# Performance work log

Hardware: AMD Instinct MI355X
Metric: run time of the kernel (lower is better)

The kernel has to match this reference:

```python
import jax, jax.numpy as jnp
import numpy as np


def setup_inputs() -> dict:
    key = jax.random.key(0)
    k1, k2, k3 = jax.random.split(key, 3)
    B, S, D, N = 2, 2048, 1024, 16
    H = D // N  # head_dim = 64
    x = jax.random.normal(k1, (B, S, D), dtype=jnp.float32)
    W_qkv = jax.random.normal(k2, (N, D, 3 * H), dtype=jnp.float32) / np.sqrt(D).astype(np.float32)
    W_out = jax.random.normal(k3, (N, H, D), dtype=jnp.float32) / np.sqrt(D).astype(np.float32)
    return {"x": x, "W_qkv": W_qkv, "W_out": W_out}


def reference(x, W_qkv, W_out):
    B, S, D = x.shape
    head_dim = W_qkv.shape[-1] // 3
    # QKV projection per head: [B, N, S, 3*H]
    qkv = jnp.einsum('bsd,ndh->bnsh', x, W_qkv)
    q, k, v = jnp.split(qkv, 3, axis=-1)  # each [B, N, S, H]
    scale = jnp.asarray(1.0 / np.sqrt(head_dim), dtype=x.dtype)
    attn = jnp.einsum('bnqh,bnkh->bnqk', q, k) * scale  # [B, N, S, S]
    # causal mask: -1e10 above the diagonal (matches buffer in original)
    mask = jnp.asarray(-1e10, dtype=x.dtype) * (1.0 - jnp.tril(jnp.ones((S, S), dtype=x.dtype)))
    attn = jax.nn.softmax(attn + mask, axis=-1)
    out = jnp.einsum('bnqk,bnkh->bnqh', attn, v)  # [B, N, S, H]
    # faithful to original: raw row-major reshape [B,N,S,H] -> [B, N*H, S]
    out = out.reshape(B, -1, S)
    # faithful to original einsum: d kept, n and h summed over W_out
    return jnp.einsum('bds,nhd->bsd', out, W_out)
```

## Files before the change

### kernel.cpp

```cpp
#include <hip/hip_runtime.h>
#include <hip/hip_bf16.h>

#define B_ 2
#define S_ 2048
#define D_ 1024
#define N_ 16
#define H_ 64

typedef unsigned short u16;
typedef unsigned int u32;
typedef __bf16 bf16x8 __attribute__((ext_vector_type(8)));
typedef u16 u16x8 __attribute__((ext_vector_type(8)));
typedef u32 u32x2 __attribute__((ext_vector_type(2)));
typedef float f4v __attribute__((ext_vector_type(4)));

__device__ __forceinline__ u16 f2b(float f) {
    u32 u = __builtin_bit_cast(u32, f);
    u32 r = (u + 0x7FFFu + ((u >> 16) & 1u)) >> 16;
    return (u16)r;
}
__device__ __forceinline__ bf16x8 asbf(u16x8 v) { return __builtin_bit_cast(bf16x8, v); }
__device__ __forceinline__ u32 cvtpk(float a, float b) {
    u32 r;
    asm("v_cvt_pk_bf16_f32 %0, %1, %2" : "=v"(r) : "v"(a), "v"(b));
    return r;
}
__device__ __forceinline__ void gload16(const u16* g, u16* l) {
    __builtin_amdgcn_global_load_lds((const __attribute__((address_space(1))) void*)g,
                                     (__attribute__((address_space(3))) void*)l, 16, 0, 0);
}

__global__ __launch_bounds__(256) void k_setup(const float* __restrict__ x,
                                               const float* __restrict__ w,
                                               const float* __restrict__ Wout,
                                               u16* __restrict__ xb,
                                               u16* __restrict__ wt,
                                               float* __restrict__ wsum) {
    __shared__ float T[64][65];
    const int bid = blockIdx.x;
    const int t = threadIdx.x;
    if (bid < 2048) {
        size_t i = ((size_t)bid * 256 + t) * 8;
        float4 f0 = *(const float4*)(x + i);
        float4 f1 = *(const float4*)(x + i + 4);
        u16x8 o;
        o[0] = f2b(f0.x); o[1] = f2b(f0.y); o[2] = f2b(f0.z); o[3] = f2b(f0.w);
        o[4] = f2b(f1.x); o[5] = f2b(f1.y); o[6] = f2b(f1.z); o[7] = f2b(f1.w);
        *(u16x8*)(xb + i) = o;
    } else if (bid < 2816) {
        const int v = bid - 2048;
        const int n = v / 48, rem = v % 48;
        const int jt = rem >> 4, d0 = (rem & 15) * 64;
        const int j0 = jt * 64;
        const float sc = (jt == 0) ? 0.125f * 1.44269504089f : 1.0f;
#pragma unroll
        for (int rep = 0; rep < 4; ++rep) {
            int vv = t + rep * 256;
            int row = vv >> 4, c4 = vv & 15;
            float4 f = *(const float4*)(w + ((size_t)(n * 1024 + d0 + row)) * 192 + j0 + c4 * 4);
            T[row][c4 * 4 + 0] = f.x * sc;
            T[row][c4 * 4 + 1] = f.y * sc;
            T[row][c4 * 4 + 2] = f.z * sc;
            T[row][c4 * 4 + 3] = f.w * sc;
        }
        __syncthreads();
#pragma unroll
        for (int rep = 0; rep < 2; ++rep) {
            int c = t + rep * 256;
            int j = c >> 3, db = c & 7;
            u16x8 o;
#pragma unroll
            for (int e = 0; e < 8; ++e) o[e] = f2b(T[db * 8 + e][j]);
            *(u16x8*)(wt + ((size_t)(n * 192 + j0 + j)) * 1024 + d0 + db * 8) = o;
        }
    } else {
        const int bx = bid - 2816;
        const int dd = t & 15, rr = t >> 4;
        const int d = bx * 16 + dd;
        float s = 0.f;
        for (int r = rr * 64; r < rr * 64 + 64; ++r) s += Wout[(size_t)r * 1024 + d];
        float* red = &T[0][0];
        red[rr * 17 + dd] = s;
        __syncthreads();
        if (rr == 0) {
            float tt = 0.f;
#pragma unroll
            for (int k = 0; k < 16; ++k) tt += red[k * 17 + dd];
            wsum[d] = tt;
        }
    }
}

__global__ __launch_bounds__(512) void k_qkv(const u16* __restrict__ xb,
                                             const u16* __restrict__ wt,
                                             u16* __restrict__ qbuf,
                                             u16* __restrict__ kbuf,
                                             u16* __restrict__ vt) {
    __shared__ u16 As[128 * 64];
    __shared__ u16 Bst[192 * 64];
    const int st = blockIdx.x, n = blockIdx.y;
    const int t = threadIdx.x;
    const int w = t >> 6, lane = t & 63, hi2 = lane >> 4, lo4 = lane & 15;
    const int wm = w >> 2, wn = w & 3;

    const int l8 = lane >> 3, l7 = (lane & 7) * 8;
    const u16* AgL = xb + (size_t)(st * 128 + w * 16 + l8) * 1024 + l7;
    u16* AdL = As + w * 16 * 64;
    const u16* BgL = wt + (size_t)(n * 192 + w * 24 + l8) * 1024 + l7;
    u16* BdL = Bst + w * 24 * 64;

    f4v acc[4][3];
#pragma unroll
    for (int i = 0; i < 4; ++i)
#pragma unroll
        for (int j = 0; j < 3; ++j) acc[i][j] = (f4v){0.f, 0.f, 0.f, 0.f};

    for (int kk = 0; kk < 16; ++kk) {
        __syncthreads();
        const int ko = kk * 64;
        gload16(AgL + ko, AdL);
        gload16(AgL + ko + (size_t)8 * 1024, AdL + 8 * 64);
        gload16(BgL + ko, BdL);
        gload16(BgL + ko + (size_t)8 * 1024, BdL + 8 * 64);
        gload16(BgL + ko + (size_t)16 * 1024, BdL + 16 * 64);
        __syncthreads();
        bf16x8 fa[4][2];
#pragma unroll
        for (int ms = 0; ms < 4; ++ms) {
            const u16* ar = As + (wm * 64 + ms * 16 + lo4) * 64;
            fa[ms][0] = asbf(*(const u16x8*)(ar + hi2 * 8));
            fa[ms][1] = asbf(*(const u16x8*)(ar + hi2 * 8 + 32));
        }
        __builtin_amdgcn_s_setprio(1);
#pragma unroll
        for (int fj = 0; fj < 3; ++fj) {
            const u16* br = Bst + (wn * 48 + fj * 16 + lo4) * 64;
            bf16x8 fb0 = asbf(*(const u16x8*)(br + hi2 * 8));
            bf16x8 fb1 = asbf(*(const u16x8*)(br + hi2 * 8 + 32));
#pragma unroll
            for (int ms = 0; ms < 4; ++ms) {
                acc[ms][fj] = __builtin_amdgcn_mfma_f32_16x16x32_bf16(fa[ms][0], fb0, acc[ms][fj], 0, 0, 0);
                acc[ms][fj] = __builtin_amdgcn_mfma_f32_16x16x32_bf16(fa[ms][1], fb1, acc[ms][fj], 0, 0, 0);
            }
        }
        __builtin_amdgcn_s_setprio(0);
    }

    const int b = st >> 4, s128 = (st & 15) * 128;
    u16* Cs = As;
#pragma unroll
    for (int sec = 0; sec < 3; ++sec) {
        __syncthreads();
#pragma unroll
        for (int fj = 0; fj < 3; ++fj) {
            const int base = wn * 48 + fj * 16;
            if ((base >> 6) == sec) {
                const int col = base - sec * 64 + lo4;
#pragma unroll
                for (int ms = 0; ms < 4; ++ms)
#pragma unroll
                    for (int r = 0; r < 4; ++r)
                        Cs[(wm * 64 + ms * 16 + hi2 * 4 + r) * 64 + col] = f2b(acc[ms][fj][r]);
            }
        }
        __syncthreads();
        if (sec == 2) {
            const int h = t & 63, sb = t >> 6;
            u16x8 o0, o1;
#pragma unroll
            for (int e = 0; e < 8; ++e) o0[e] = Cs[(sb * 16 + e) * 64 + h];
#pragma unroll
            for (int e = 0; e < 8; ++e) o1[e] = Cs[(sb * 16 + 8 + e) * 64 + h];
            u16* dst = vt + ((size_t)(b * 16 + n) * 64 + h) * 2048 + s128 + sb * 16;
            *(u16x8*)dst = o0;
            *(u16x8*)(dst + 8) = o1;
        } else {
            const int row = t >> 2, off = (t & 3) * 16;
            u16* dst = (sec == 0) ? qbuf : kbuf;
            dst += ((size_t)(b * 16 + n) * 2048 + s128 + row) * 64 + off;
            *(u16x8*)dst = *(const u16x8*)(Cs + row * 64 + off);
            *(u16x8*)(dst + 8) = *(const u16x8*)(Cs + row * 64 + off + 8);
        }
    }
}

__global__ __launch_bounds__(512) void k_attn(const u16* __restrict__ qbuf,
                                              const u16* __restrict__ kbuf,
                                              const u16* __restrict__ vt,
                                              const float* __restrict__ wsum,
                                              float* __restrict__ out) {
    __shared__ u16 SMEM[24576];
    u16* Ks = SMEM;
    u16* Vs = SMEM + 8192;
    u16* Ps = SMEM + 16384;
    const int id = blockIdx.x;
    const int bn = id & 31;
    const int qx = id >> 5;
    const int qb = (qx < 8) ? (15 - 2 * qx) : (2 * (qx - 8));
    const int t = threadIdx.x;
    const int w = t >> 6, lane = t & 63, hi2 = lane >> 4, lo4 = lane & 15;

    const int q = qb * 128 + w * 16 + lo4;
    const u16* Qp = qbuf + ((size_t)bn * 2048 + q) * 64;
    bf16x8 bq0 = asbf(*(const u16x8*)(Qp + hi2 * 8));
    bf16x8 bq1 = asbf(*(const u16x8*)(Qp + 32 + hi2 * 8));

    const int srow = t >> 3, so = t & 7;
    const u16* Kg = kbuf + (size_t)bn * 2048 * 64 + (size_t)srow * 64 + so * 8;
    const u16* Vg = vt + (size_t)bn * 64 * 2048 + (size_t)srow * 2048 + so * 8;
    const int soff = srow * 64 + ((so * 8) ^ ((srow & 7) << 3));

    f4v accO[4];
#pragma unroll
    for (int i = 0; i < 4; ++i) accO[i] = (f4v){0.f, 0.f, 0.f, 0.f};
    float l = 0.f;

    const int rsw = (lo4 & 7) << 3;
    u16* Pw = Ps + w * 1024 + lo4 * 64;
    const int npair = qb + 1;

    u16x8 krA = *(const u16x8*)(Kg);
    u16x8 krB = *(const u16x8*)(Kg + 4096);
    u16x8 vrA = *(const u16x8*)(Vg);
    u16x8 vrB = *(const u16x8*)(Vg + 64);

    for (int pair = 0; pair < npair; ++pair) {
        __syncthreads();
        *(u16x8*)(Ks + soff) = krA;
        *(u16x8*)(Ks + 4096 + soff) = krB;
        *(u16x8*)(Vs + soff) = vrA;
        *(u16x8*)(Vs + 4096 + soff) = vrB;
        if (pair + 1 < npair) {
            const size_t ko = (size_t)(pair + 1) * 8192;
            krA = *(const u16x8*)(Kg + ko);
            krB = *(const u16x8*)(Kg + ko + 4096);
            vrA = *(const u16x8*)(Vg + (pair + 1) * 128);
            vrB = *(const u16x8*)(Vg + (pair + 1) * 128 + 64);
        }
        __syncthreads();

#pragma unroll
        for (int sub = 0; sub < 2; ++sub) {
            const int kb = 2 * pair + sub;
            const u16* Kc = Ks + sub * 4096;
            const u16* Vc = Vs + sub * 4096;

            f4v s4[4];
#pragma unroll
            for (int i = 0; i < 4; ++i) s4[i] = (f4v){0.f, 0.f, 0.f, 0.f};
            __builtin_amdgcn_s_setprio(1);
#pragma unroll
            for (int fi = 0; fi < 4; ++fi) {
                const u16* kr = Kc + (fi * 16 + lo4) * 64;
                bf16x8 ka0 = asbf(*(const u16x8*)(kr + ((hi2 * 8) ^ rsw)));
                bf16x8 ka1 = asbf(*(const u16x8*)(kr + ((hi2 * 8 + 32) ^ rsw)));
                s4[fi] = __builtin_amdgcn_mfma_f32_16x16x32_bf16(ka0, bq0, s4[fi], 0, 0, 0);
                s4[fi] = __builtin_amdgcn_mfma_f32_16x16x32_bf16(ka1, bq1, s4[fi], 0, 0, 0);
            }
            __builtin_amdgcn_s_setprio(0);

            if (kb >= 2 * qb) {
#pragma unroll
                for (int fi = 0; fi < 4; ++fi)
#pragma unroll
                    for (int r = 0; r < 4; ++r) {
                        int kvg = kb * 64 + fi * 16 + hi2 * 4 + r;
                        if (kvg > q) s4[fi][r] = -3.0e38f;
                    }
            }

#pragma unroll
            for (int fi = 0; fi < 4; ++fi) {
#pragma unroll
                for (int r = 0; r < 4; ++r) {
                    float pv = __builtin_exp2f(s4[fi][r]);
                    s4[fi][r] = pv;
                    l += pv;
                }
                u32x2 pk;
                pk[0] = cvtpk(s4[fi][0], s4[fi][1]);
                pk[1] = cvtpk(s4[fi][2], s4[fi][3]);
                *(u32x2*)(Pw + ((fi * 16 + hi2 * 4) ^ rsw)) = pk;
            }

            bf16x8 pb0 = asbf(*(const u16x8*)(Pw + ((hi2 * 8) ^ rsw)));
            bf16x8 pb1 = asbf(*(const u16x8*)(Pw + ((32 + hi2 * 8) ^ rsw)));
            __builtin_amdgcn_s_setprio(1);
#pragma unroll
            for (int fh = 0; fh < 4; ++fh) {
                const u16* vr = Vc + (fh * 16 + lo4) * 64;
                bf16x8 va0 = asbf(*(const u16x8*)(vr + ((hi2 * 8) ^ rsw)));
                bf16x8 va1 = asbf(*(const u16x8*)(vr + ((hi2 * 8 + 32) ^ rsw)));
                accO[fh] = __builtin_amdgcn_mfma_f32_16x16x32_bf16(va0, pb0, accO[fh], 0, 0, 0);
                accO[fh] = __builtin_amdgcn_mfma_f32_16x16x32_bf16(va1, pb1, accO[fh], 0, 0, 0);
            }
            __builtin_amdgcn_s_setprio(0);
        }
    }

    l += __shfl_xor(l, 16);
    l += __shfl_xor(l, 32);

    __syncthreads();
    float* Osh = (float*)SMEM;
    {
        float inv = 1.f / l;
        const int orl = w * 16 + lo4;
        const int osw = (lo4 & 7) << 2;
        float* Or = Osh + orl * 64;
#pragma unroll
        for (int fh = 0; fh < 4; ++fh) {
            f4v o;
#pragma unroll
            for (int r = 0; r < 4; ++r) o[r] = accO[fh][r] * inv;
            *(f4v*)(Or + ((fh * 16 + hi2 * 4) ^ osw)) = o;
        }
    }
    __syncthreads();
    {
        const int b = bn >> 4, n = bn & 15;
        const int d0 = n * 64 + qb * 4;
        float4 wv = *(const float4*)(wsum + d0);
#pragma unroll
        for (int rep = 0; rep < 4; ++rep) {
            int p = rep * 512 + t;
            int h = p & 63, tt = p >> 6;
            const int key = (tt & 7) << 2;
            const int hc = h ^ key;
            float4 o;
            o.x = Osh[(tt)*64 + hc] * wv.x;
            o.y = Osh[(32 + tt) * 64 + hc] * wv.y;
            o.z = Osh[(64 + tt) * 64 + hc] * wv.z;
            o.w = Osh[(96 + tt) * 64 + hc] * wv.w;
            *(float4*)(out + ((size_t)b * 2048 + p) * 1024 + d0) = o;
        }
    }
}

extern "C" void kernel_launch(void* const* d_in, const int* in_sizes, int n_in,
                              void* d_out, int out_size, void* d_ws, size_t ws_size,
                              hipStream_t stream) {
    const float* x = (const float*)d_in[0];
    const float* Wqkv = (const float*)d_in[1];
    const float* Wout = (const float*)d_in[2];
    float* out = (float*)d_out;

    char* p = (char*)d_ws;
    float* wsum = (float*)p; p += 4096;
    u16* xb = (u16*)p; p += (size_t)4096 * 1024 * 2;
    u16* wt = (u16*)p; p += (size_t)16 * 192 * 1024 * 2;
    u16* qb_ = (u16*)p; p += (size_t)32 * 2048 * 64 * 2;
    u16* kb_ = (u16*)p; p += (size_t)32 * 2048 * 64 * 2;
    u16* vt_ = (u16*)p; p += (size_t)32 * 2048 * 64 * 2;

    k_setup<<<2880, 256, 0, stream>>>(x, Wqkv, Wout, xb, wt, wsum);
    k_qkv<<<dim3(32, 16), 512, 0, stream>>>(xb, wt, qb_, kb_, vt_);
    k_attn<<<512, 512, 0, stream>>>(qb_, kb_, vt_, wsum, out);
}
```

Before: 88.78 us.

## Split attention KV sub-tiles across two wave groups with 1024-thread blocks

Doubles the attention block to 1024 threads so that each 64-key sub-tile of a 128-key pair goes to its own group of 8 waves, instead of one wave handling both sub-tiles in sequence. The two partial outputs and row sums are combined through shared memory before normalization. Each thread now does one K and one V global load per pair. This shortens the serial chain per wave and adds parallelism, at the cost of more registers per block, a larger LDS footprint, and an extra reduction step.

```diff
diff --git a/kernel.cpp b/kernel.cpp
--- a/kernel.cpp
+++ b/kernel.cpp
@@ -184,12 +184,12 @@
     }
 }
 
-__global__ __launch_bounds__(512) void k_attn(const u16* __restrict__ qbuf,
-                                              const u16* __restrict__ kbuf,
-                                              const u16* __restrict__ vt,
-                                              const float* __restrict__ wsum,
-                                              float* __restrict__ out) {
-    __shared__ u16 SMEM[24576];
+__global__ __launch_bounds__(1024) void k_attn(const u16* __restrict__ qbuf,
+                                               const u16* __restrict__ kbuf,
+                                               const u16* __restrict__ vt,
+                                               const float* __restrict__ wsum,
+                                               float* __restrict__ out) {
+    __shared__ u16 SMEM[32768];
     u16* Ks = SMEM;
     u16* Vs = SMEM + 8192;
     u16* Ps = SMEM + 16384;
@@ -199,16 +199,20 @@
     const int qb = (qx < 8) ? (15 - 2 * qx) : (2 * (qx - 8));
     const int t = threadIdx.x;
     const int w = t >> 6, lane = t & 63, hi2 = lane >> 4, lo4 = lane & 15;
-
-    const int q = qb * 128 + w * 16 + lo4;
+    const int wq = w & 7, par = w >> 3;
+
+    const int q = qb * 128 + wq * 16 + lo4;
     const u16* Qp = qbuf + ((size_t)bn * 2048 + q) * 64;
     bf16x8 bq0 = asbf(*(const u16x8*)(Qp + hi2 * 8));
     bf16x8 bq1 = asbf(*(const u16x8*)(Qp + 32 + hi2 * 8));
 
-    const int srow = t >> 3, so = t & 7;
-    const u16* Kg = kbuf + (size_t)bn * 2048 * 64 + (size_t)srow * 64 + so * 8;
-    const u16* Vg = vt + (size_t)bn * 64 * 2048 + (size_t)srow * 2048 + so * 8;
-    const int soff = srow * 64 + ((so * 8) ^ ((srow & 7) << 3));
+    const int prow = t >> 3, so = t & 7;
+    const int stile = prow >> 6, srw = prow & 63;
+    const u16* Kg = kbuf + (size_t)bn * 131072 + (size_t)prow * 64 + so * 8;
+    const u16* Vg = vt + (size_t)bn * 131072 + (size_t)srw * 2048 + stile * 64 + so * 8;
+    const int ssw = (srw & 7) << 3;
+    u16* Kl = Ks + stile * 4096 + srw * 64 + ((so * 8) ^ ssw);
+    u16* Vl = Vs + stile * 4096 + srw * 64 + ((so * 8) ^ ssw);
 
     f4v accO[4];
 #pragma unroll
@@ -219,83 +223,73 @@
     u16* Pw = Ps + w * 1024 + lo4 * 64;
     const int npair = qb + 1;
 
-    u16x8 krA = *(const u16x8*)(Kg);
-    u16x8 krB = *(const u16x8*)(Kg + 4096);
-    u16x8 vrA = *(const u16x8*)(Vg);
-    u16x8 vrB = *(const u16x8*)(Vg + 64);
+    u16x8 kr = *(const u16x8*)(Kg);
+    u16x8 vr = *(const u16x8*)(Vg);
 
     for (int pair = 0; pair < npair; ++pair) {
         __syncthreads();
-        *(u16x8*)(Ks + soff) = krA;
-        *(u16x8*)(Ks + 4096 + soff) = krB;
-        *(u16x8*)(Vs + soff) = vrA;
-        *(u16x8*)(Vs + 4096 + soff) = vrB;
+        *(u16x8*)Kl = kr;
+        *(u16x8*)Vl = vr;
         if (pair + 1 < npair) {
-            const size_t ko = (size_t)(pair + 1) * 8192;
-            krA = *(const u16x8*)(Kg + ko);
-            krB = *(const u16x8*)(Kg + ko + 4096);
-            vrA = *(const u16x8*)(Vg + (pair + 1) * 128);
-            vrB = *(const u16x8*)(Vg + (pair + 1) * 128 + 64);
-        }
-        __syncthreads();
-
-#pragma unroll
-        for (int sub = 0; sub < 2; ++sub) {
-            const int kb = 2 * pair + sub;
-            const u16* Kc = Ks + sub * 4096;
-            const u16* Vc = Vs + sub * 4096;
-
-            f4v s4[4];
-#pragma unroll
-            for (int i = 0; i < 4; ++i) s4[i] = (f4v){0.f, 0.f, 0.f, 0.f};
-            __builtin_amdgcn_s_setprio(1);
-#pragma unroll
-            for (int fi = 0; fi < 4; ++fi) {
-                const u16* kr = Kc + (fi * 16 + lo4) * 64;
-                bf16x8 ka0 = asbf(*(const u16x8*)(kr + ((hi2 * 8) ^ rsw)));
-                bf16x8 ka1 = asbf(*(const u16x8*)(kr + ((hi2 * 8 + 32) ^ rsw)));
-                s4[fi] = __builtin_amdgcn_mfma_f32_16x16x32_bf16(ka0, bq0, s4[fi], 0, 0, 0);
-                s4[fi] = __builtin_amdgcn_mfma_f32_16x16x32_bf16(ka1, bq1, s4[fi], 0, 0, 0);
+            kr = *(const u16x8*)(Kg + (size_t)(pair + 1) * 8192);
+            vr = *(const u16x8*)(Vg + (pair + 1) * 128);
+        }
+        __syncthreads();
+
+        const int kb = 2 * pair + par;
+        const u16* Kc = Ks + par * 4096;
+        const u16* Vc = Vs + par * 4096;
+
+        f4v s4[4];
+#pragma unroll
+        for (int i = 0; i < 4; ++i) s4[i] = (f4v){0.f, 0.f, 0.f, 0.f};
+        __builtin_amdgcn_s_setprio(1);
+#pragma unroll
+        for (int fi = 0; fi < 4; ++fi) {
+            const u16* krw = Kc + (fi * 16 + lo4) * 64;
+            bf16x8 ka0 = asbf(*(const u16x8*)(krw + ((hi2 * 8) ^ rsw)));
+            bf16x8 ka1 = asbf(*(const u16x8*)(krw + ((hi2 * 8 + 32) ^ rsw)));
+            s4[fi] = __builtin_amdgcn_mfma_f32_16x16x32_bf16(ka0, bq0, s4[fi], 0, 0, 0);
+            s4[fi] = __builtin_amdgcn_mfma_f32_16x16x32_bf16(ka1, bq1, s4[fi], 0, 0, 0);
+        }
+        __builtin_amdgcn_s_setprio(0);
+
+        if (kb >= 2 * qb) {
+#pragma unroll
+            for (int fi = 0; fi < 4; ++fi)
+#pragma unroll
+                for (int r = 0; r < 4; ++r) {
+                    int kvg = kb * 64 + fi * 16 + hi2 * 4 + r;
+                    if (kvg > q) s4[fi][r] = -3.0e38f;
+                }
+        }
+
+#pragma unroll
+        for (int fi = 0; fi < 4; ++fi) {
+#pragma unroll
+            for (int r = 0; r < 4; ++r) {
+                float pv = __builtin_exp2f(s4[fi][r]);
+                s4[fi][r] = pv;
+                l += pv;
             }
-            __builtin_amdgcn_s_setprio(0);
-
-            if (kb >= 2 * qb) {
-#pragma unroll
-                for (int fi = 0; fi < 4; ++fi)
-#pragma unroll
-                    for (int r = 0; r < 4; ++r) {
-                        int kvg = kb * 64 + fi * 16 + hi2 * 4 + r;
-                        if (kvg > q) s4[fi][r] = -3.0e38f;
-                    }
-            }
-
-#pragma unroll
-            for (int fi = 0; fi < 4; ++fi) {
-#pragma unroll
-                for (int r = 0; r < 4; ++r) {
-                    float pv = __builtin_exp2f(s4[fi][r]);
-                    s4[fi][r] = pv;
-                    l += pv;
-                }
-                u32x2 pk;
-                pk[0] = cvtpk(s4[fi][0], s4[fi][1]);
-                pk[1] = cvtpk(s4[fi][2], s4[fi][3]);
-                *(u32x2*)(Pw + ((fi * 16 + hi2 * 4) ^ rsw)) = pk;
-            }
-
-            bf16x8 pb0 = asbf(*(const u16x8*)(Pw + ((hi2 * 8) ^ rsw)));
-            bf16x8 pb1 = asbf(*(const u16x8*)(Pw + ((32 + hi2 * 8) ^ rsw)));
-            __builtin_amdgcn_s_setprio(1);
-#pragma unroll
-            for (int fh = 0; fh < 4; ++fh) {
-                const u16* vr = Vc + (fh * 16 + lo4) * 64;
-                bf16x8 va0 = asbf(*(const u16x8*)(vr + ((hi2 * 8) ^ rsw)));
-                bf16x8 va1 = asbf(*(const u16x8*)(vr + ((hi2 * 8 + 32) ^ rsw)));
-                accO[fh] = __builtin_amdgcn_mfma_f32_16x16x32_bf16(va0, pb0, accO[fh], 0, 0, 0);
-                accO[fh] = __builtin_amdgcn_mfma_f32_16x16x32_bf16(va1, pb1, accO[fh], 0, 0, 0);
-            }
-            __builtin_amdgcn_s_setprio(0);
-        }
+            u32x2 pk;
+            pk[0] = cvtpk(s4[fi][0], s4[fi][1]);
+            pk[1] = cvtpk(s4[fi][2], s4[fi][3]);
+            *(u32x2*)(Pw + ((fi * 16 + hi2 * 4) ^ rsw)) = pk;
+        }
+
+        bf16x8 pb0 = asbf(*(const u16x8*)(Pw + ((hi2 * 8) ^ rsw)));
+        bf16x8 pb1 = asbf(*(const u16x8*)(Pw + ((32 + hi2 * 8) ^ rsw)));
+        __builtin_amdgcn_s_setprio(1);
+#pragma unroll
+        for (int fh = 0; fh < 4; ++fh) {
+            const u16* vrw = Vc + (fh * 16 + lo4) * 64;
+            bf16x8 va0 = asbf(*(const u16x8*)(vrw + ((hi2 * 8) ^ rsw)));
+            bf16x8 va1 = asbf(*(const u16x8*)(vrw + ((hi2 * 8 + 32) ^ rsw)));
+            accO[fh] = __builtin_amdgcn_mfma_f32_16x16x32_bf16(va0, pb0, accO[fh], 0, 0, 0);
+            accO[fh] = __builtin_amdgcn_mfma_f32_16x16x32_bf16(va1, pb1, accO[fh], 0, 0, 0);
+        }
+        __builtin_amdgcn_s_setprio(0);
     }
 
     l += __shfl_xor(l, 16);
@@ -303,17 +297,26 @@
 
     __syncthreads();
     float* Osh = (float*)SMEM;
-    {
-        float inv = 1.f / l;
-        const int orl = w * 16 + lo4;
-        const int osw = (lo4 & 7) << 2;
-        float* Or = Osh + orl * 64;
+    float* lsh = (float*)(SMEM + 16384);
+    const int orl = wq * 16 + lo4;
+    const int osw = (lo4 & 7) << 2;
+    float* Or = Osh + orl * 64;
+    if (par == 0) {
+#pragma unroll
+        for (int fh = 0; fh < 4; ++fh)
+            *(f4v*)(Or + ((fh * 16 + hi2 * 4) ^ osw)) = accO[fh];
+        if (hi2 == 0) lsh[orl] = l;
+    }
+    __syncthreads();
+    if (par == 1) {
+        float inv = 1.f / (l + lsh[orl]);
 #pragma unroll
         for (int fh = 0; fh < 4; ++fh) {
-            f4v o;
-#pragma unroll
-            for (int r = 0; r < 4; ++r) o[r] = accO[fh][r] * inv;
-            *(f4v*)(Or + ((fh * 16 + hi2 * 4) ^ osw)) = o;
+            float* addr = Or + ((fh * 16 + hi2 * 4) ^ osw);
+            f4v o = *(f4v*)addr;
+#pragma unroll
+            for (int r = 0; r < 4; ++r) o[r] = (o[r] + accO[fh][r]) * inv;
+            *(f4v*)addr = o;
         }
     }
     __syncthreads();
@@ -322,8 +325,8 @@
         const int d0 = n * 64 + qb * 4;
         float4 wv = *(const float4*)(wsum + d0);
 #pragma unroll
-        for (int rep = 0; rep < 4; ++rep) {
-            int p = rep * 512 + t;
+        for (int rep = 0; rep < 2; ++rep) {
+            int p = rep * 1024 + t;
             int h = p & 63, tt = p >> 6;
             const int key = (tt & 7) << 2;
             const int hc = h ^ key;
@@ -355,5 +358,5 @@
 
     k_setup<<<2880, 256, 0, stream>>>(x, Wqkv, Wout, xb, wt, wsum);
     k_qkv<<<dim3(32, 16), 512, 0, stream>>>(xb, wt, qb_, kb_, vt_);
-    k_attn<<<512, 512, 0, stream>>>(qb_, kb_, vt_, wsum, out);
-}
+    k_attn<<<512, 1024, 0, stream>>>(qb_, kb_, vt_, wsum, out);
+}
```

After: 104.0 us. 17.2% more time.

## Process two query row-groups per wave in attention to reuse K/V fragments

Applied to the files above, without the earlier changes.

The attention kernel drops from 8 to 4 waves per block, and each wave now handles 32 query rows (two 16-row groups) instead of 16. Each K and V fragment read from LDS is reused for two MFMAs, which halves LDS read traffic per MFMA. The K/V global-to-LDS staging is remapped so 256 threads each load four 16-byte chunks. The cost is doubled accumulator and score registers per wave and fewer waves per block to hide latency.

```diff
diff --git a/kernel.cpp b/kernel.cpp
--- a/kernel.cpp
+++ b/kernel.cpp
@@ -184,7 +184,7 @@
     }
 }
 
-__global__ __launch_bounds__(512) void k_attn(const u16* __restrict__ qbuf,
+__global__ __launch_bounds__(256) void k_attn(const u16* __restrict__ qbuf,
                                               const u16* __restrict__ kbuf,
                                               const u16* __restrict__ vt,
                                               const float* __restrict__ wsum,
@@ -200,42 +200,57 @@
     const int t = threadIdx.x;
     const int w = t >> 6, lane = t & 63, hi2 = lane >> 4, lo4 = lane & 15;
 
-    const int q = qb * 128 + w * 16 + lo4;
-    const u16* Qp = qbuf + ((size_t)bn * 2048 + q) * 64;
-    bf16x8 bq0 = asbf(*(const u16x8*)(Qp + hi2 * 8));
-    bf16x8 bq1 = asbf(*(const u16x8*)(Qp + 32 + hi2 * 8));
-
-    const int srow = t >> 3, so = t & 7;
-    const u16* Kg = kbuf + (size_t)bn * 2048 * 64 + (size_t)srow * 64 + so * 8;
-    const u16* Vg = vt + (size_t)bn * 64 * 2048 + (size_t)srow * 2048 + so * 8;
-    const int soff = srow * 64 + ((so * 8) ^ ((srow & 7) << 3));
-
-    f4v accO[4];
-#pragma unroll
-    for (int i = 0; i < 4; ++i) accO[i] = (f4v){0.f, 0.f, 0.f, 0.f};
-    float l = 0.f;
+    bf16x8 bq[2][2];
+#pragma unroll
+    for (int g = 0; g < 2; ++g) {
+        const u16* Qp = qbuf + ((size_t)bn * 2048 + qb * 128 + w * 32 + g * 16 + lo4) * 64;
+        bq[g][0] = asbf(*(const u16x8*)(Qp + hi2 * 8));
+        bq[g][1] = asbf(*(const u16x8*)(Qp + 32 + hi2 * 8));
+    }
+    const int q0 = qb * 128 + w * 32 + lo4;
+
+    const int stile = t >> 7, srw = (t >> 1) & 63, shalf = t & 1;
+    const u16* Kg = kbuf + (size_t)bn * 131072 + (size_t)(stile * 64 + srw) * 64 + shalf * 32;
+    const u16* Vg = vt + (size_t)bn * 131072 + (size_t)srw * 2048 + stile * 64 + shalf * 32;
+    const int ssw = (srw & 7) << 3;
+    u16* Kl = Ks + stile * 4096 + srw * 64;
+    u16* Vl = Vs + stile * 4096 + srw * 64;
+    int sco[4];
+#pragma unroll
+    for (int c = 0; c < 4; ++c) sco[c] = (shalf * 32 + c * 8) ^ ssw;
+
+    f4v accO[2][4];
+#pragma unroll
+    for (int g = 0; g < 2; ++g)
+#pragma unroll
+        for (int i = 0; i < 4; ++i) accO[g][i] = (f4v){0.f, 0.f, 0.f, 0.f};
+    float l2[2] = {0.f, 0.f};
 
     const int rsw = (lo4 & 7) << 3;
-    u16* Pw = Ps + w * 1024 + lo4 * 64;
     const int npair = qb + 1;
 
-    u16x8 krA = *(const u16x8*)(Kg);
-    u16x8 krB = *(const u16x8*)(Kg + 4096);
-    u16x8 vrA = *(const u16x8*)(Vg);
-    u16x8 vrB = *(const u16x8*)(Vg + 64);
+    u16x8 kr[4], vr[4];
+#pragma unroll
+    for (int c = 0; c < 4; ++c) {
+        kr[c] = *(const u16x8*)(Kg + c * 8);
+        vr[c] = *(const u16x8*)(Vg + c * 8);
+    }
 
     for (int pair = 0; pair < npair; ++pair) {
         __syncthreads();
-        *(u16x8*)(Ks + soff) = krA;
-        *(u16x8*)(Ks + 4096 + soff) = krB;
-        *(u16x8*)(Vs + soff) = vrA;
-        *(u16x8*)(Vs + 4096 + soff) = vrB;
+#pragma unroll
+        for (int c = 0; c < 4; ++c) {
+            *(u16x8*)(Kl + sco[c]) = kr[c];
+            *(u16x8*)(Vl + sco[c]) = vr[c];
+        }
         if (pair + 1 < npair) {
             const size_t ko = (size_t)(pair + 1) * 8192;
-            krA = *(const u16x8*)(Kg + ko);
-            krB = *(const u16x8*)(Kg + ko + 4096);
-            vrA = *(const u16x8*)(Vg + (pair + 1) * 128);
-            vrB = *(const u16x8*)(Vg + (pair + 1) * 128 + 64);
+            const int vo = (pair + 1) * 128;
+#pragma unroll
+            for (int c = 0; c < 4; ++c) {
+                kr[c] = *(const u16x8*)(Kg + ko + c * 8);
+                vr[c] = *(const u16x8*)(Vg + vo + c * 8);
+            }
         }
         __syncthreads();
 
@@ -245,74 +260,95 @@
             const u16* Kc = Ks + sub * 4096;
             const u16* Vc = Vs + sub * 4096;
 
-            f4v s4[4];
-#pragma unroll
-            for (int i = 0; i < 4; ++i) s4[i] = (f4v){0.f, 0.f, 0.f, 0.f};
+            f4v s4[2][4];
+#pragma unroll
+            for (int g = 0; g < 2; ++g)
+#pragma unroll
+                for (int i = 0; i < 4; ++i) s4[g][i] = (f4v){0.f, 0.f, 0.f, 0.f};
             __builtin_amdgcn_s_setprio(1);
 #pragma unroll
             for (int fi = 0; fi < 4; ++fi) {
-                const u16* kr = Kc + (fi * 16 + lo4) * 64;
-                bf16x8 ka0 = asbf(*(const u16x8*)(kr + ((hi2 * 8) ^ rsw)));
-                bf16x8 ka1 = asbf(*(const u16x8*)(kr + ((hi2 * 8 + 32) ^ rsw)));
-                s4[fi] = __builtin_amdgcn_mfma_f32_16x16x32_bf16(ka0, bq0, s4[fi], 0, 0, 0);
-                s4[fi] = __builtin_amdgcn_mfma_f32_16x16x32_bf16(ka1, bq1, s4[fi], 0, 0, 0);
+                const u16* krw = Kc + (fi * 16 + lo4) * 64;
+                bf16x8 ka0 = asbf(*(const u16x8*)(krw + ((hi2 * 8) ^ rsw)));
+                bf16x8 ka1 = asbf(*(const u16x8*)(krw + ((hi2 * 8 + 32) ^ rsw)));
+#pragma unroll
+                for (int g = 0; g < 2; ++g) {
+                    s4[g][fi] = __builtin_amdgcn_mfma_f32_16x16x32_bf16(ka0, bq[g][0], s4[g][fi], 0, 0, 0);
+                    s4[g][fi] = __builtin_amdgcn_mfma_f32_16x16x32_bf16(ka1, bq[g][1], s4[g][fi], 0, 0, 0);
+                }
             }
             __builtin_amdgcn_s_setprio(0);
 
             if (kb >= 2 * qb) {
 #pragma unroll
-                for (int fi = 0; fi < 4; ++fi)
+                for (int g = 0; g < 2; ++g) {
+                    const int qg = q0 + g * 16;
+#pragma unroll
+                    for (int fi = 0; fi < 4; ++fi)
+#pragma unroll
+                        for (int r = 0; r < 4; ++r) {
+                            int kvg = kb * 64 + fi * 16 + hi2 * 4 + r;
+                            if (kvg > qg) s4[g][fi][r] = -3.0e38f;
+                        }
+                }
+            }
+
+            bf16x8 pb[2][2];
+#pragma unroll
+            for (int g = 0; g < 2; ++g) {
+                u16* Pw = Ps + (w * 2 + g) * 1024 + lo4 * 64;
+#pragma unroll
+                for (int fi = 0; fi < 4; ++fi) {
 #pragma unroll
                     for (int r = 0; r < 4; ++r) {
-                        int kvg = kb * 64 + fi * 16 + hi2 * 4 + r;
-                        if (kvg > q) s4[fi][r] = -3.0e38f;
+                        float pv = __builtin_exp2f(s4[g][fi][r]);
+                        s4[g][fi][r] = pv;
+                        l2[g] += pv;
                     }
-            }
-
-#pragma unroll
-            for (int fi = 0; fi < 4; ++fi) {
-#pragma unroll
-                for (int r = 0; r < 4; ++r) {
-                    float pv = __builtin_exp2f(s4[fi][r]);
-                    s4[fi][r] = pv;
-                    l += pv;
+                    u32x2 pk;
+                    pk[0] = cvtpk(s4[g][fi][0], s4[g][fi][1]);
+                    pk[1] = cvtpk(s4[g][fi][2], s4[g][fi][3]);
+                    *(u32x2*)(Pw + ((fi * 16 + hi2 * 4) ^ rsw)) = pk;
                 }
-                u32x2 pk;
-                pk[0] = cvtpk(s4[fi][0], s4[fi][1]);
-                pk[1] = cvtpk(s4[fi][2], s4[fi][3]);
-                *(u32x2*)(Pw + ((fi * 16 + hi2 * 4) ^ rsw)) = pk;
-            }
-
-            bf16x8 pb0 = asbf(*(const u16x8*)(Pw + ((hi2 * 8) ^ rsw)));
-            bf16x8 pb1 = asbf(*(const u16x8*)(Pw + ((32 + hi2 * 8) ^ rsw)));
+                pb[g][0] = asbf(*(const u16x8*)(Pw + ((hi2 * 8) ^ rsw)));
+                pb[g][1] = asbf(*(const u16x8*)(Pw + ((32 + hi2 * 8) ^ rsw)));
+            }
+
             __builtin_amdgcn_s_setprio(1);
 #pragma unroll
             for (int fh = 0; fh < 4; ++fh) {
-                const u16* vr = Vc + (fh * 16 + lo4) * 64;
-                bf16x8 va0 = asbf(*(const u16x8*)(vr + ((hi2 * 8) ^ rsw)));
-                bf16x8 va1 = asbf(*(const u16x8*)(vr + ((hi2 * 8 + 32) ^ rsw)));
-                accO[fh] = __builtin_amdgcn_mfma_f32_16x16x32_bf16(va0, pb0, accO[fh], 0, 0, 0);
-                accO[fh] = __builtin_amdgcn_mfma_f32_16x16x32_bf16(va1, pb1, accO[fh], 0, 0, 0);
+                const u16* vrw = Vc + (fh * 16 + lo4) * 64;
+                bf16x8 va0 = asbf(*(const u16x8*)(vrw + ((hi2 * 8) ^ rsw)));
+                bf16x8 va1 = asbf(*(const u16x8*)(vrw + ((hi2 * 8 + 32) ^ rsw)));
+#pragma unroll
+                for (int g = 0; g < 2; ++g) {
+                    accO[g][fh] = __builtin_amdgcn_mfma_f32_16x16x32_bf16(va0, pb[g][0], accO[g][fh], 0, 0, 0);
+                    accO[g][fh] = __builtin_amdgcn_mfma_f32_16x16x32_bf16(va1, pb[g][1], accO[g][fh], 0, 0, 0);
+                }
             }
             __builtin_amdgcn_s_setprio(0);
         }
     }
 
-    l += __shfl_xor(l, 16);
-    l += __shfl_xor(l, 32);
+#pragma unroll
+    for (int g = 0; g < 2; ++g) {
+        l2[g] += __shfl_xor(l2[g], 16);
+        l2[g] += __shfl_xor(l2[g], 32);
+    }
 
     __syncthreads();
     float* Osh = (float*)SMEM;
-    {
-        float inv = 1.f / l;
-        const int orl = w * 16 + lo4;
+#pragma unroll
+    for (int g = 0; g < 2; ++g) {
+        float inv = 1.f / l2[g];
+        const int orl = w * 32 + g * 16 + lo4;
         const int osw = (lo4 & 7) << 2;
         float* Or = Osh + orl * 64;
 #pragma unroll
         for (int fh = 0; fh < 4; ++fh) {
             f4v o;
 #pragma unroll
-            for (int r = 0; r < 4; ++r) o[r] = accO[fh][r] * inv;
+            for (int r = 0; r < 4; ++r) o[r] = accO[g][fh][r] * inv;
             *(f4v*)(Or + ((fh * 16 + hi2 * 4) ^ osw)) = o;
         }
     }
@@ -322,8 +358,8 @@
         const int d0 = n * 64 + qb * 4;
         float4 wv = *(const float4*)(wsum + d0);
 #pragma unroll
-        for (int rep = 0; rep < 4; ++rep) {
-            int p = rep * 512 + t;
+        for (int rep = 0; rep < 8; ++rep) {
+            int p = rep * 256 + t;
             int h = p & 63, tt = p >> 6;
             const int key = (tt & 7) << 2;
             const int hc = h ^ key;
@@ -355,5 +391,5 @@
 
     k_setup<<<2880, 256, 0, stream>>>(x, Wqkv, Wout, xb, wt, wsum);
     k_qkv<<<dim3(32, 16), 512, 0, stream>>>(xb, wt, qb_, kb_, vt_);
-    k_attn<<<512, 512, 0, stream>>>(qb_, kb_, vt_, wsum, out);
-}
+    k_attn<<<512, 256, 0, stream>>>(qb_, kb_, vt_, wsum, out);
+}
```

After: 97.86 us. +10.2%, slower.

## Keep softmax probabilities in registers by permuting V columns in shared memory

Applied to the files above, without the earlier changes.

Drops the per-warp shared-memory round trip for the probability tile. The exp'd scores are packed directly into bf16 MFMA operands, and the V tile is stored in shared memory with a permuted column order so the key index in each lane's register fragment matches. This removes LDS writes and reads plus the extra shared buffer, shrinking LDS use per block. In exchange, V stores become narrower 8-byte writes, which may cost more store instructions or bank conflicts.

```diff
diff --git a/kernel.cpp b/kernel.cpp
--- a/kernel.cpp
+++ b/kernel.cpp
@@ -12,6 +12,7 @@
 typedef __bf16 bf16x8 __attribute__((ext_vector_type(8)));
 typedef u16 u16x8 __attribute__((ext_vector_type(8)));
 typedef u32 u32x2 __attribute__((ext_vector_type(2)));
+typedef u32 u32x4 __attribute__((ext_vector_type(4)));
 typedef float f4v __attribute__((ext_vector_type(4)));
 
 __device__ __forceinline__ u16 f2b(float f) {
@@ -189,10 +190,9 @@
                                               const u16* __restrict__ vt,
                                               const float* __restrict__ wsum,
                                               float* __restrict__ out) {
-    __shared__ u16 SMEM[24576];
+    __shared__ u16 SMEM[16384];
     u16* Ks = SMEM;
     u16* Vs = SMEM + 8192;
-    u16* Ps = SMEM + 16384;
     const int id = blockIdx.x;
     const int bn = id & 31;
     const int qx = id >> 5;
@@ -208,7 +208,11 @@
     const int srow = t >> 3, so = t & 7;
     const u16* Kg = kbuf + (size_t)bn * 2048 * 64 + (size_t)srow * 64 + so * 8;
     const u16* Vg = vt + (size_t)bn * 64 * 2048 + (size_t)srow * 2048 + so * 8;
-    const int soff = srow * 64 + ((so * 8) ^ ((srow & 7) << 3));
+    const int ssw = (srow & 7) << 3;
+    const int ksoff = srow * 64 + ((so * 8) ^ ssw);
+    const int vsb = 32 * (so >> 2) + 16 * (so & 1) + 4 * ((so >> 1) & 1);
+    const int vo0 = srow * 64 + ((vsb + 0) ^ ssw);
+    const int vo1 = srow * 64 + ((vsb + 8) ^ ssw);
 
     f4v accO[4];
 #pragma unroll
@@ -216,7 +220,6 @@
     float l = 0.f;
 
     const int rsw = (lo4 & 7) << 3;
-    u16* Pw = Ps + w * 1024 + lo4 * 64;
     const int npair = qb + 1;
 
     u16x8 krA = *(const u16x8*)(Kg);
@@ -226,10 +229,16 @@
 
     for (int pair = 0; pair < npair; ++pair) {
         __syncthreads();
-        *(u16x8*)(Ks + soff) = krA;
-        *(u16x8*)(Ks + 4096 + soff) = krB;
-        *(u16x8*)(Vs + soff) = vrA;
-        *(u16x8*)(Vs + 4096 + soff) = vrB;
+        *(u16x8*)(Ks + ksoff) = krA;
+        *(u16x8*)(Ks + 4096 + ksoff) = krB;
+        {
+            u32x4 va = __builtin_bit_cast(u32x4, vrA);
+            u32x4 vb = __builtin_bit_cast(u32x4, vrB);
+            *(u32x2*)(Vs + vo0) = (u32x2){va[0], va[1]};
+            *(u32x2*)(Vs + vo1) = (u32x2){va[2], va[3]};
+            *(u32x2*)(Vs + 4096 + vo0) = (u32x2){vb[0], vb[1]};
+            *(u32x2*)(Vs + 4096 + vo1) = (u32x2){vb[2], vb[3]};
+        }
         if (pair + 1 < npair) {
             const size_t ko = (size_t)(pair + 1) * 8192;
             krA = *(const u16x8*)(Kg + ko);
@@ -270,27 +279,27 @@
             }
 
 #pragma unroll
-            for (int fi = 0; fi < 4; ++fi) {
+            for (int fi = 0; fi < 4; ++fi)
 #pragma unroll
                 for (int r = 0; r < 4; ++r) {
                     float pv = __builtin_exp2f(s4[fi][r]);
                     s4[fi][r] = pv;
                     l += pv;
                 }
-                u32x2 pk;
-                pk[0] = cvtpk(s4[fi][0], s4[fi][1]);
-                pk[1] = cvtpk(s4[fi][2], s4[fi][3]);
-                *(u32x2*)(Pw + ((fi * 16 + hi2 * 4) ^ rsw)) = pk;
-            }
-
-            bf16x8 pb0 = asbf(*(const u16x8*)(Pw + ((hi2 * 8) ^ rsw)));
-            bf16x8 pb1 = asbf(*(const u16x8*)(Pw + ((32 + hi2 * 8) ^ rsw)));
+
+            u32x4 p0 = {cvtpk(s4[0][0], s4[0][1]), cvtpk(s4[0][2], s4[0][3]),
+                        cvtpk(s4[1][0], s4[1][1]), cvtpk(s4[1][2], s4[1][3])};
+            u32x4 p1 = {cvtpk(s4[2][0], s4[2][1]), cvtpk(s4[2][2], s4[2][3]),
+                        cvtpk(s4[3][0], s4[3][1]), cvtpk(s4[3][2], s4[3][3])};
+            bf16x8 pb0 = __builtin_bit_cast(bf16x8, p0);
+            bf16x8 pb1 = __builtin_bit_cast(bf16x8, p1);
+
             __builtin_amdgcn_s_setprio(1);
 #pragma unroll
             for (int fh = 0; fh < 4; ++fh) {
-                const u16* vr = Vc + (fh * 16 + lo4) * 64;
-                bf16x8 va0 = asbf(*(const u16x8*)(vr + ((hi2 * 8) ^ rsw)));
-                bf16x8 va1 = asbf(*(const u16x8*)(vr + ((hi2 * 8 + 32) ^ rsw)));
+                const u16* vrw = Vc + (fh * 16 + lo4) * 64;
+                bf16x8 va0 = asbf(*(const u16x8*)(vrw + ((hi2 * 8) ^ rsw)));
+                bf16x8 va1 = asbf(*(const u16x8*)(vrw + ((32 + hi2 * 8) ^ rsw)));
                 accO[fh] = __builtin_amdgcn_mfma_f32_16x16x32_bf16(va0, pb0, accO[fh], 0, 0, 0);
                 accO[fh] = __builtin_amdgcn_mfma_f32_16x16x32_bf16(va1, pb1, accO[fh], 0, 0, 0);
             }
```

Result: no change. 88.82 us (+0.0%).
